# Kernel tuning notes

Measured on AMD Instinct MI355X. Metric: run time of the kernel, lower is better.

## Reference

```python
import jax, jax.numpy as jnp
import numpy as np

BASIS_ORDER = 7  # basis_dim = 8 (Chebyshev T_0..T_7 of tanh(x))


def chebyshev_basis(x, order=BASIS_ORDER):
    """x: [batch, in] -> [batch, in, order+1] Chebyshev basis on tanh(x)."""
    xt = jnp.tanh(x)
    terms = [jnp.ones_like(xt), xt]
    for _ in range(2, order + 1):
        terms.append(2.0 * xt * terms[-1] - terms[-2])
    return jnp.stack(terms[: order + 1], axis=-1)


def setup_inputs() -> dict:
    key = jax.random.key(0)
    k1, k2, k3 = jax.random.split(key, 3)
    batch, in_f, out_f, K = 4096, 1024, 1024, BASIS_ORDER + 1
    x = jax.random.normal(k1, (batch, in_f), dtype=jnp.float32)
    # Kaiming-uniform-ish init scale
    bound = 1.0 / np.sqrt(in_f * K)
    weights = jax.random.uniform(k2, (out_f, in_f, K), dtype=jnp.float32,
                                 minval=-bound, maxval=bound)
    bias_param = jax.random.uniform(k3, (out_f,), dtype=jnp.float32,
                                    minval=-bound, maxval=bound)
    return {"x": x, "weights": weights, "bias_param": bias_param}


def reference(x, weights, bias_param):
    # basis: [b, i, k]; weights: [o, i, k] -> out[b, o] = sum_{i,k} basis*W
    basis = chebyshev_basis(x)  # [batch, in, K]
    out = jnp.einsum('bik,oik->bo', basis, weights)
    return out + bias_param
```

## Files before the change

kernel.cpp:

```cpp
#include <hip/hip_runtime.h>
#include <hip/hip_bf16.h>

#define MD 4096
#define ND 1024
#define KD 8192
#define IN_F 1024

typedef __bf16 bf16x8 __attribute__((ext_vector_type(8)));
typedef float f32x4 __attribute__((ext_vector_type(4)));

#define N_BASIS (MD * IN_F)
#define N_CONV ((ND * KD) / 8)

__global__ __launch_bounds__(256) void prep_kernel(
    const float* __restrict__ x, const float* __restrict__ w,
    __bf16* __restrict__ A, __bf16* __restrict__ B) {
  int i = blockIdx.x * blockDim.x + threadIdx.x;
  if (i < N_BASIS) {
    float t = tanhf(x[i]);
    float two_t = 2.0f * t;
    float T0 = 1.0f;
    float T1 = t;
    float T2 = two_t * T1 - T0;
    float T3 = two_t * T2 - T1;
    float T4 = two_t * T3 - T2;
    float T5 = two_t * T4 - T3;
    float T6 = two_t * T5 - T4;
    float T7 = two_t * T6 - T5;
    bf16x8 v;
    v[0] = (__bf16)T0; v[1] = (__bf16)T1; v[2] = (__bf16)T2; v[3] = (__bf16)T3;
    v[4] = (__bf16)T4; v[5] = (__bf16)T5; v[6] = (__bf16)T6; v[7] = (__bf16)T7;
    *(bf16x8*)(A + (size_t)i * 8) = v;
  } else if (i < N_BASIS + N_CONV) {
    int j = i - N_BASIS;
    const float4* p = (const float4*)(w + (size_t)j * 8);
    float4 a = p[0], b = p[1];
    bf16x8 v;
    v[0] = (__bf16)a.x; v[1] = (__bf16)a.y; v[2] = (__bf16)a.z; v[3] = (__bf16)a.w;
    v[4] = (__bf16)b.x; v[5] = (__bf16)b.y; v[6] = (__bf16)b.z; v[7] = (__bf16)b.w;
    *(bf16x8*)(B + (size_t)j * 8) = v;
  }
}

#define BM 128
#define BN 128
#define BK 64
#define KHALF 4096
#define NTH (KHALF / BK)
#define TSZ (BM * BK)

__global__ __launch_bounds__(256) void gemm_bias(
    const __bf16* __restrict__ A, const __bf16* __restrict__ B,
    const float* __restrict__ bias, float* __restrict__ C,
    float* __restrict__ P1) {
  __shared__ __align__(16) __bf16 As[TSZ];
  __shared__ __align__(16) __bf16 Bs[TSZ];

  const int tid = threadIdx.x;
  const int wave = tid >> 6;
  const int lane = tid & 63;

  const int b = blockIdx.x;
  const int xcd = b & 7;
  const int j = b >> 3;
  const int nt = j & 7;
  const int kh = (j >> 3) & 1;
  const int mloc = j >> 4;
  const int n0 = nt * BN;
  const int m0 = (xcd * 4 + mloc) * BM;
  const size_t k0 = (size_t)kh * KHALF;

  const int wm = wave >> 1;
  const int wn = wave & 1;

  const int ar = lane >> 3;
  const int swz_col = ((lane & 7) ^ ar) * 8;
  const __bf16* gA = A + (size_t)(m0 + wave * 32 + ar) * KD + k0 + swz_col;
  const __bf16* gB = B + (size_t)(n0 + wave * 32 + ar) * KD + k0 + swz_col;
  const int loff = wave * 32 * BK;

  f32x4 acc[4][4];
#pragma unroll
  for (int i = 0; i < 4; i++)
#pragma unroll
    for (int jj = 0; jj < 4; jj++) acc[i][jj] = (f32x4){0.f, 0.f, 0.f, 0.f};

  const int fr = lane & 15;
  const int fr7 = fr & 7;
  const int qk = lane >> 4;

  for (int kt = 0; kt < KHALF; kt += BK) {
#pragma unroll
    for (int jj = 0; jj < 4; jj++) {
      __builtin_amdgcn_global_load_lds(
          (const __attribute__((address_space(1))) void*)(gA + kt + (size_t)jj * 8 * KD),
          (__attribute__((address_space(3))) void*)(&As[loff + jj * 8 * BK]), 16, 0, 0);
      __builtin_amdgcn_global_load_lds(
          (const __attribute__((address_space(1))) void*)(gB + kt + (size_t)jj * 8 * KD),
          (__attribute__((address_space(3))) void*)(&Bs[loff + jj * 8 * BK]), 16, 0, 0);
    }
    __syncthreads();

#pragma unroll
    for (int s = 0; s < 2; s++) {
      const int pa = ((s * 4 + qk) ^ fr7) * 8;
      bf16x8 af[4], bfr[4];
#pragma unroll
      for (int mi = 0; mi < 4; mi++)
        af[mi] = *(const bf16x8*)&As[(wm * 64 + mi * 16 + fr) * BK + pa];
#pragma unroll
      for (int ni = 0; ni < 4; ni++)
        bfr[ni] = *(const bf16x8*)&Bs[(wn * 64 + ni * 16 + fr) * BK + pa];
#pragma unroll
      for (int mi = 0; mi < 4; mi++)
#pragma unroll
        for (int ni = 0; ni < 4; ni++)
          acc[mi][ni] = __builtin_amdgcn_mfma_f32_16x16x32_bf16(
              af[mi], bfr[ni], acc[mi][ni], 0, 0, 0);
    }
    __syncthreads();
  }

  float* dst = kh ? P1 : C;
  const int col0 = n0 + wn * 64;
  const int row0 = m0 + wm * 64 + qk * 4;
#pragma unroll
  for (int ni = 0; ni < 4; ni++) {
    int col = col0 + ni * 16 + fr;
    float bv = kh ? 0.0f : bias[col];
#pragma unroll
    for (int mi = 0; mi < 4; mi++) {
      int row = row0 + mi * 16;
#pragma unroll
      for (int r = 0; r < 4; r++)
        dst[(size_t)(row + r) * ND + col] = acc[mi][ni][r] + bv;
    }
  }
}

__global__ __launch_bounds__(256) void reduce_kernel(
    float* __restrict__ C, const float* __restrict__ P1) {
  size_t i = (size_t)blockIdx.x * blockDim.x + threadIdx.x;
  f32x4 c = ((const f32x4*)C)[i];
  f32x4 p = ((const f32x4*)P1)[i];
#pragma unroll
  for (int r = 0; r < 4; r++) c[r] += p[r];
  ((f32x4*)C)[i] = c;
}

extern "C" void kernel_launch(void* const* d_in, const int* in_sizes, int n_in,
                              void* d_out, int out_size, void* d_ws, size_t ws_size,
                              hipStream_t stream) {
  const float* x = (const float*)d_in[0];
  const float* w = (const float*)d_in[1];
  const float* bias = (const float*)d_in[2];
  float* out = (float*)d_out;

  __bf16* Abf = (__bf16*)d_ws;
  __bf16* Bbf = (__bf16*)((char*)d_ws + (size_t)MD * KD * 2);
  float* P1 = (float*)((char*)d_ws + (size_t)MD * KD * 2 + (size_t)ND * KD * 2);

  {
    int n = N_BASIS + N_CONV;
    prep_kernel<<<(n + 255) / 256, 256, 0, stream>>>(x, w, Abf, Bbf);
  }
  {
    gemm_bias<<<512, 256, 0, stream>>>(Abf, Bbf, bias, out, P1);
  }
  {
    reduce_kernel<<<(MD * ND) / 4 / 256, 256, 0, stream>>>(out, P1);
  }
}
```

Before: 179.0 us.

## Move split-K into the block with 8 waves and reduce through LDS

The two K halves are now computed by two groups of four waves inside one 512-thread block instead of by separate blocks. The second half's accumulators are staged through shared memory and added in the epilogue together with the bias. This removes the separate reduce kernel and the partial-sum buffer's global writes and reads. The staging buffer spans 64KB starting at As, so it assumes As and Bs are laid out contiguously in shared memory. Launch bounds now request higher occupancy with the larger block.

```diff
diff --git a/kernel.cpp b/kernel.cpp
--- a/kernel.cpp
+++ b/kernel.cpp
@@ -46,38 +46,37 @@
 #define BN 128
 #define BK 64
 #define KHALF 4096
-#define NTH (KHALF / BK)
 #define TSZ (BM * BK)
 
-__global__ __launch_bounds__(256) void gemm_bias(
+__global__ __launch_bounds__(512, 4) void gemm_bias(
     const __bf16* __restrict__ A, const __bf16* __restrict__ B,
-    const float* __restrict__ bias, float* __restrict__ C,
-    float* __restrict__ P1) {
-  __shared__ __align__(16) __bf16 As[TSZ];
-  __shared__ __align__(16) __bf16 Bs[TSZ];
+    const float* __restrict__ bias, float* __restrict__ C) {
+  __shared__ __align__(16) __bf16 As[2][TSZ];
+  __shared__ __align__(16) __bf16 Bs[2][TSZ];
 
   const int tid = threadIdx.x;
   const int wave = tid >> 6;
+  const int kh = wave >> 2;
+  const int w4 = wave & 3;
   const int lane = tid & 63;
 
   const int b = blockIdx.x;
   const int xcd = b & 7;
   const int j = b >> 3;
   const int nt = j & 7;
-  const int kh = (j >> 3) & 1;
-  const int mloc = j >> 4;
+  const int mloc = j >> 3;
   const int n0 = nt * BN;
   const int m0 = (xcd * 4 + mloc) * BM;
   const size_t k0 = (size_t)kh * KHALF;
 
-  const int wm = wave >> 1;
-  const int wn = wave & 1;
+  const int wm = w4 >> 1;
+  const int wn = w4 & 1;
 
   const int ar = lane >> 3;
   const int swz_col = ((lane & 7) ^ ar) * 8;
-  const __bf16* gA = A + (size_t)(m0 + wave * 32 + ar) * KD + k0 + swz_col;
-  const __bf16* gB = B + (size_t)(n0 + wave * 32 + ar) * KD + k0 + swz_col;
-  const int loff = wave * 32 * BK;
+  const __bf16* gA = A + (size_t)(m0 + w4 * 32 + ar) * KD + k0 + swz_col;
+  const __bf16* gB = B + (size_t)(n0 + w4 * 32 + ar) * KD + k0 + swz_col;
+  const int loff = w4 * 32 * BK;
 
   f32x4 acc[4][4];
 #pragma unroll
@@ -94,10 +93,10 @@
     for (int jj = 0; jj < 4; jj++) {
       __builtin_amdgcn_global_load_lds(
           (const __attribute__((address_space(1))) void*)(gA + kt + (size_t)jj * 8 * KD),
-          (__attribute__((address_space(3))) void*)(&As[loff + jj * 8 * BK]), 16, 0, 0);
+          (__attribute__((address_space(3))) void*)(&As[kh][loff + jj * 8 * BK]), 16, 0, 0);
       __builtin_amdgcn_global_load_lds(
           (const __attribute__((address_space(1))) void*)(gB + kt + (size_t)jj * 8 * KD),
-          (__attribute__((address_space(3))) void*)(&Bs[loff + jj * 8 * BK]), 16, 0, 0);
+          (__attribute__((address_space(3))) void*)(&Bs[kh][loff + jj * 8 * BK]), 16, 0, 0);
     }
     __syncthreads();
 
@@ -107,10 +106,10 @@
       bf16x8 af[4], bfr[4];
 #pragma unroll
       for (int mi = 0; mi < 4; mi++)
-        af[mi] = *(const bf16x8*)&As[(wm * 64 + mi * 16 + fr) * BK + pa];
+        af[mi] = *(const bf16x8*)&As[kh][(wm * 64 + mi * 16 + fr) * BK + pa];
 #pragma unroll
       for (int ni = 0; ni < 4; ni++)
-        bfr[ni] = *(const bf16x8*)&Bs[(wn * 64 + ni * 16 + fr) * BK + pa];
+        bfr[ni] = *(const bf16x8*)&Bs[kh][(wn * 64 + ni * 16 + fr) * BK + pa];
 #pragma unroll
       for (int mi = 0; mi < 4; mi++)
 #pragma unroll
@@ -121,31 +120,32 @@
     __syncthreads();
   }
 
-  float* dst = kh ? P1 : C;
-  const int col0 = n0 + wn * 64;
-  const int row0 = m0 + wm * 64 + qk * 4;
+  float* M = (float*)&As[0][0];
+  if (kh == 1) {
 #pragma unroll
-  for (int ni = 0; ni < 4; ni++) {
-    int col = col0 + ni * 16 + fr;
-    float bv = kh ? 0.0f : bias[col];
+    for (int mi = 0; mi < 4; mi++)
 #pragma unroll
-    for (int mi = 0; mi < 4; mi++) {
-      int row = row0 + mi * 16;
+      for (int ni = 0; ni < 4; ni++)
+        *(f32x4*)&M[((w4 * 16 + mi * 4 + ni) * 64 + lane) * 4] = acc[mi][ni];
+  }
+  __syncthreads();
+  if (kh == 0) {
+    const int col0 = n0 + wn * 64;
+    const int row0 = m0 + wm * 64 + qk * 4;
 #pragma unroll
-      for (int r = 0; r < 4; r++)
-        dst[(size_t)(row + r) * ND + col] = acc[mi][ni][r] + bv;
+    for (int ni = 0; ni < 4; ni++) {
+      int col = col0 + ni * 16 + fr;
+      float bv = bias[col];
+#pragma unroll
+      for (int mi = 0; mi < 4; mi++) {
+        f32x4 other = *(const f32x4*)&M[((w4 * 16 + mi * 4 + ni) * 64 + lane) * 4];
+        int row = row0 + mi * 16;
+#pragma unroll
+        for (int r = 0; r < 4; r++)
+          C[(size_t)(row + r) * ND + col] = acc[mi][ni][r] + other[r] + bv;
+      }
     }
   }
-}
-
-__global__ __launch_bounds__(256) void reduce_kernel(
-    float* __restrict__ C, const float* __restrict__ P1) {
-  size_t i = (size_t)blockIdx.x * blockDim.x + threadIdx.x;
-  f32x4 c = ((const f32x4*)C)[i];
-  f32x4 p = ((const f32x4*)P1)[i];
-#pragma unroll
-  for (int r = 0; r < 4; r++) c[r] += p[r];
-  ((f32x4*)C)[i] = c;
 }
 
 extern "C" void kernel_launch(void* const* d_in, const int* in_sizes, int n_in,
@@ -158,16 +158,12 @@
 
   __bf16* Abf = (__bf16*)d_ws;
   __bf16* Bbf = (__bf16*)((char*)d_ws + (size_t)MD * KD * 2);
-  float* P1 = (float*)((char*)d_ws + (size_t)MD * KD * 2 + (size_t)ND * KD * 2);
 
   {
     int n = N_BASIS + N_CONV;
     prep_kernel<<<(n + 255) / 256, 256, 0, stream>>>(x, w, Abf, Bbf);
   }
   {
-    gemm_bias<<<512, 256, 0, stream>>>(Abf, Bbf, bias, out, P1);
-  }
-  {
-    reduce_kernel<<<(MD * ND) / 4 / 256, 256, 0, stream>>>(out, P1);
+    gemm_bias<<<256, 512, 0, stream>>>(Abf, Bbf, bias, out);
   }
 }
```

Measured after the change: 193.5 us. +8.1%, slower.
